# Kernel tuning notes

Hardware: AMD Instinct MI355X
Metric: run time of the kernel (lower is better)

## Reference

```python
import jax, jax.numpy as jnp
import numpy as np

N = 8192
D = 64  # node feature width
E = 64  # edge-derived feature width


def setup_inputs() -> dict:
    key = jax.random.key(0)
    k1, k2, k3 = jax.random.split(key, 3)
    # Dense normalized adjacency (module stores normalize(A).toarray()); values in [0,1).
    A = jax.random.uniform(k1, (N, N), dtype=jnp.float32) / N  # scaled like a normalized adjacency
    F = jax.random.normal(k2, (N, D), dtype=jnp.float32)
    new_features = jax.random.normal(k3, (N, E), dtype=jnp.float32)
    return {"A": A, "F": F, "new_features": new_features}


def reference(A, F, new_features):
    # layer 1: node branch gets ReLU, edge-feature branch does not
    h = jax.nn.relu(A @ F)              # [N, D]
    g = A @ new_features                # [N, E]
    # layer 2
    h = jax.nn.relu(A @ h)              # [N, D]
    g = A @ g                           # [N, E]
    return jnp.concatenate([h, g], axis=-1)  # [N, D+E]
```

## Files before the change

kernel.cpp:

```cpp
#include <hip/hip_runtime.h>
#include <hip/hip_bf16.h>


typedef unsigned short ushort_t;
typedef __attribute__((ext_vector_type(8))) short short8;
typedef __attribute__((ext_vector_type(4))) float f32x4;
typedef __attribute__((ext_vector_type(4))) unsigned short us4;

#define NN 8192
#define NO 128
#define NSPLIT 8
#define KSPAN 1024
#define KSTEPS 32

__global__ void detect_dtype(const ushort_t* __restrict__ A, int* __restrict__ flag) {
  __shared__ int smax, szero;
  const int t = threadIdx.x;
  if (t == 0) { smax = 0; szero = 0; }
  __syncthreads();
  int lmax = 0, lzero = 0;
  #pragma unroll
  for (int j = 0; j < 8; ++j) {
    int idx = t * 8 + j;
    int u = (int)A[idx];
    if ((idx & 1) == 0) {
      lmax = max(lmax, u);
      lzero += (u == 0) ? 1 : 0;
    }
  }
  atomicMax(&smax, lmax);
  atomicAdd(&szero, lzero);
  __syncthreads();
  if (t == 0) *flag = (smax > 0x3A00 || szero > 800) ? 1 : 0;
}

__global__ void zero_ws(float* __restrict__ p) {
  size_t i = ((size_t)blockIdx.x * 256 + threadIdx.x) * 4;
  *(float4*)(p + i) = make_float4(0.f, 0.f, 0.f, 0.f);
}

__device__ __forceinline__ short bf16bits(float x) {
  __hip_bfloat16 h = __float2bfloat16(x);
  return *reinterpret_cast<short*>(&h);
}

__device__ __forceinline__ short8 cvt8(float4 a, float4 b) {
  short8 r;
  r[0] = bf16bits(a.x); r[1] = bf16bits(a.y); r[2] = bf16bits(a.z); r[3] = bf16bits(a.w);
  r[4] = bf16bits(b.x); r[5] = bf16bits(b.y); r[6] = bf16bits(b.z); r[7] = bf16bits(b.w);
  return r;
}

__global__ void pack_b(const ushort_t* __restrict__ F, const ushort_t* __restrict__ NF,
                       ushort_t* __restrict__ Bpk, const int* __restrict__ flag) {
  int gid = blockIdx.x * 256 + threadIdx.x;
  int l = gid & 63, ks = (gid >> 6) & 255, nt = gid >> 14;
  int n = nt * 16 + (l & 15);
  int k0 = ks * 32 + (l >> 4) * 8;
  ushort_t* dst = Bpk + (((size_t)nt * 256 + ks) << 9) + l * 8;
  short8 v;
  if (*flag) {
    const float* src = (n < 64) ? ((const float*)F + n) : ((const float*)NF + n - 64);
    #pragma unroll
    for (int j = 0; j < 8; ++j) v[j] = bf16bits(src[(size_t)(k0 + j) << 6]);
  } else {
    const ushort_t* src = (n < 64) ? (F + n) : (NF + n - 64);
    #pragma unroll
    for (int j = 0; j < 8; ++j) v[j] = (short)src[(size_t)(k0 + j) << 6];
  }
  *(short8*)dst = v;
}

__global__ __launch_bounds__(256) void gemm(
    const ushort_t* __restrict__ Au, const float* __restrict__ Af,
    ushort_t* __restrict__ Apk, const ushort_t* __restrict__ Bpk,
    float* __restrict__ P, const int* __restrict__ flag, int wb, int usepk) {
  __shared__ __align__(16) ushort_t lsA[4 * 512];
  const int t = threadIdx.x;
  const int w = t >> 6, lane = t & 63;
  const int mblk = blockIdx.x >> 3;
  const int split = blockIdx.x & 7;
  const size_t m0 = (size_t)mblk * 64;
  const int ks0 = split * KSTEPS;
  const int l15 = lane & 15, lq = lane >> 4;
  const int fl = *flag;

  const f32x4 zero = {0.f, 0.f, 0.f, 0.f};
  f32x4 acc[8];
  #pragma unroll
  for (int nt = 0; nt < 8; ++nt) acc[nt] = zero;

  if (usepk && fl) {
    const ushort_t* ap = Apk + (((size_t)(mblk * 4 + w) * 256 + ks0) << 9) + lane * 8;
    const ushort_t* bp = Bpk + ((size_t)ks0 << 9) + lane * 8;
    #pragma unroll 2
    for (int it = 0; it < KSTEPS; ++it) {
      short8 a = *(const short8*)ap;
      #pragma unroll
      for (int nt = 0; nt < 8; ++nt) {
        short8 b = *(const short8*)(bp + ((size_t)nt << 17));
        acc[nt] = __builtin_amdgcn_mfma_f32_16x16x32_bf16(a, b, acc[nt], 0, 0, 0);
      }
      ap += 512; bp += 512;
    }
  } else {
    const int r = t >> 2, cq = t & 3;
    const int mt = r >> 4;
    const int li = (r & 15) + cq * 16;
    const float*    ap_f = Af + (m0 + r) * NN + (size_t)ks0 * 32 + cq * 8;
    const ushort_t* ap_b = Au + (m0 + r) * NN + (size_t)ks0 * 32 + cq * 8;
    ushort_t* wp = Apk + (((size_t)(mblk * 4 + mt) * 256 + ks0) << 9) + li * 8;
    ushort_t* lw = lsA + mt * 512 + li * 8;
    const ushort_t* lr = lsA + w * 512 + lane * 8;
    const int dowb = wb && fl;
    for (int it = 0; it < KSTEPS; ++it) {
      short8 c;
      if (fl) {
        float4 x0 = *(const float4*)ap_f;
        float4 x1 = *(const float4*)(ap_f + 4);
        c = cvt8(x0, x1);
        ap_f += 32;
      } else {
        c = *(const short8*)ap_b;
        ap_b += 32;
      }
      if (dowb) { *(short8*)wp = c; wp += 512; }
      const ushort_t* bit = Bpk + ((size_t)(ks0 + it) << 9) + lane * 8;
      __syncthreads();
      *(short8*)lw = c;
      __syncthreads();
      short8 a = *(const short8*)lr;
      #pragma unroll
      for (int nt = 0; nt < 8; ++nt) {
        short8 b = *(const short8*)(bit + ((size_t)nt << 17));
        acc[nt] = __builtin_amdgcn_mfma_f32_16x16x32_bf16(a, b, acc[nt], 0, 0, 0);
      }
    }
  }

  const size_t mrow = m0 + w * 16 + lq * 4;
  #pragma unroll
  for (int nt = 0; nt < 8; ++nt) {
    #pragma unroll
    for (int reg = 0; reg < 4; ++reg) {
      unsafeAtomicAdd(&P[(mrow + reg) * NO + nt * 16 + l15], acc[nt][reg]);
    }
  }
}

__global__ void epi_pack(const float* __restrict__ P, ushort_t* __restrict__ Bpk2) {
  __shared__ ushort_t lt[64 * 130];
  const int t = threadIdx.x;
  const int blk = blockIdx.x;
  const size_t base = (size_t)blk * 64 * NO;
  #pragma unroll
  for (int i = 0; i < 8; ++i) {
    int e4 = (i * 256 + t) * 4;
    int m = e4 >> 7, n = e4 & 127;
    float4 v = *(const float4*)(P + base + e4);
    float s[4] = {v.x, v.y, v.z, v.w};
    if (n < 64) {
      #pragma unroll
      for (int j = 0; j < 4; ++j) s[j] = fmaxf(s[j], 0.f);
    }
    #pragma unroll
    for (int j = 0; j < 4; ++j) lt[m * 130 + n + j] = (ushort_t)bf16bits(s[j]);
  }
  __syncthreads();
  #pragma unroll
  for (int i = 0; i < 4; ++i) {
    int item = i * 256 + t;
    int l = item & 63, s = (item >> 6) & 1, nt = item >> 7;
    short8 v;
    #pragma unroll
    for (int j = 0; j < 8; ++j)
      v[j] = (short)lt[(s * 32 + (l >> 4) * 8 + j) * 130 + nt * 16 + (l & 15)];
    *(short8*)(Bpk2 + (((size_t)nt * 256 + blk * 2 + s) << 9) + l * 8) = v;
  }
}

__global__ void epi_out(const float* __restrict__ P, ushort_t* __restrict__ outb,
                        float* __restrict__ outf, const int* __restrict__ flag) {
  int idx = blockIdx.x * 256 + threadIdx.x;
  size_t e = (size_t)idx * 4;
  float4 v = *(const float4*)(P + e);
  float s[4] = {v.x, v.y, v.z, v.w};
  int n0 = (int)(e & 127);
  #pragma unroll
  for (int j = 0; j < 4; ++j) if (n0 + j < 64) s[j] = fmaxf(s[j], 0.f);
  if (*flag) {
    *(float4*)(outf + e) = make_float4(s[0], s[1], s[2], s[3]);
  } else {
    us4 r;
    #pragma unroll
    for (int j = 0; j < 4; ++j) r[j] = (ushort_t)bf16bits(s[j]);
    *(us4*)(outb + e) = r;
  }
}

extern "C" void kernel_launch(void* const* d_in, const int* in_sizes, int n_in,
                              void* d_out, int out_size, void* d_ws, size_t ws_size,
                              hipStream_t stream) {
  const ushort_t* A  = (const ushort_t*)d_in[0];
  const ushort_t* F  = (const ushort_t*)d_in[1];
  const ushort_t* NF = (const ushort_t*)d_in[2];

  char* ws = (char*)d_ws;
  ushort_t* Bpk1 = (ushort_t*)(ws);
  ushort_t* Bpk2 = (ushort_t*)(ws + (2u << 20));
  float*    P1   = (float*)(ws + (4u << 20));
  float*    P2   = (float*)(ws + (8u << 20));
  int*      flag = (int*)(ws + (12u << 20));
  ushort_t* Apk  = (ushort_t*)(ws + (16u << 20));

  const int wsok = (ws_size >= ((size_t)144 << 20) + 4) ? 1 : 0;

  detect_dtype<<<1, 256, 0, stream>>>(A, flag);
  zero_ws<<<2048, 256, 0, stream>>>(P1);
  pack_b<<<512, 256, 0, stream>>>(F, NF, Bpk1, flag);
  gemm<<<1024, 256, 0, stream>>>(A, (const float*)A, Apk, Bpk1, P1, flag,
                                 wsok, 0);
  epi_pack<<<128, 256, 0, stream>>>(P1, Bpk2);
  gemm<<<1024, 256, 0, stream>>>(A, (const float*)A, Apk, Bpk2, P2, flag,
                                 0, wsok);
  epi_out<<<1024, 256, 0, stream>>>(P2, (ushort_t*)d_out, (float*)d_out, flag);
}
```

Baseline: 514.2 us.

## Fuse split-K reduction and epilogues into GEMM via in-block LDS reduction

Each block now owns 16 output rows, and its four waves split K among themselves instead of spreading split-K across blocks. Partial results are reduced in shared memory rather than with global float atomics. The ReLU, bf16 packing for the second layer, and the final output write move into the GEMM epilogue, which removes the zero, epi_pack and epi_out launches and the fp32 partial buffers. The A tile is staged per wave in 64KB of swizzled LDS. The large LDS footprint limits occupancy, and the grid shrinks to 512 blocks.

After: 505.5 us. Within noise of the previous version (-1.7%).

```diff
diff --git a/kernel.cpp b/kernel.cpp
--- a/kernel.cpp
+++ b/kernel.cpp
@@ -9,9 +9,6 @@
 
 #define NN 8192
 #define NO 128
-#define NSPLIT 8
-#define KSPAN 1024
-#define KSTEPS 32
 
 __global__ void detect_dtype(const ushort_t* __restrict__ A, int* __restrict__ flag) {
   __shared__ int smax, szero;
@@ -34,21 +31,9 @@
   if (t == 0) *flag = (smax > 0x3A00 || szero > 800) ? 1 : 0;
 }
 
-__global__ void zero_ws(float* __restrict__ p) {
-  size_t i = ((size_t)blockIdx.x * 256 + threadIdx.x) * 4;
-  *(float4*)(p + i) = make_float4(0.f, 0.f, 0.f, 0.f);
-}
-
 __device__ __forceinline__ short bf16bits(float x) {
   __hip_bfloat16 h = __float2bfloat16(x);
   return *reinterpret_cast<short*>(&h);
-}
-
-__device__ __forceinline__ short8 cvt8(float4 a, float4 b) {
-  short8 r;
-  r[0] = bf16bits(a.x); r[1] = bf16bits(a.y); r[2] = bf16bits(a.z); r[3] = bf16bits(a.w);
-  r[4] = bf16bits(b.x); r[5] = bf16bits(b.y); r[6] = bf16bits(b.z); r[7] = bf16bits(b.w);
-  return r;
 }
 
 __global__ void pack_b(const ushort_t* __restrict__ F, const ushort_t* __restrict__ NF,
@@ -74,14 +59,13 @@
 __global__ __launch_bounds__(256) void gemm(
     const ushort_t* __restrict__ Au, const float* __restrict__ Af,
     ushort_t* __restrict__ Apk, const ushort_t* __restrict__ Bpk,
-    float* __restrict__ P, const int* __restrict__ flag, int wb, int usepk) {
-  __shared__ __align__(16) ushort_t lsA[4 * 512];
+    ushort_t* __restrict__ Bpk2, ushort_t* __restrict__ outb,
+    float* __restrict__ outf, const int* __restrict__ flag,
+    int wb, int usepk, int outmode) {
+  __shared__ __align__(16) char lds[65536];
   const int t = threadIdx.x;
   const int w = t >> 6, lane = t & 63;
-  const int mblk = blockIdx.x >> 3;
-  const int split = blockIdx.x & 7;
-  const size_t m0 = (size_t)mblk * 64;
-  const int ks0 = split * KSTEPS;
+  const int b = blockIdx.x;
   const int l15 = lane & 15, lq = lane >> 4;
   const int fl = *flag;
 
@@ -91,110 +75,104 @@
   for (int nt = 0; nt < 8; ++nt) acc[nt] = zero;
 
   if (usepk && fl) {
-    const ushort_t* ap = Apk + (((size_t)(mblk * 4 + w) * 256 + ks0) << 9) + lane * 8;
-    const ushort_t* bp = Bpk + ((size_t)ks0 << 9) + lane * 8;
+    const ushort_t* ap = Apk + (((size_t)b * 256 + w * 64) << 9) + lane * 8;
+    const ushort_t* bp = Bpk + (((size_t)w * 64) << 9) + lane * 8;
     #pragma unroll 2
-    for (int it = 0; it < KSTEPS; ++it) {
-      short8 a = *(const short8*)ap;
+    for (int kk = 0; kk < 64; ++kk) {
+      short8 a = *(const short8*)(ap + ((size_t)kk << 9));
       #pragma unroll
       for (int nt = 0; nt < 8; ++nt) {
-        short8 b = *(const short8*)(bp + ((size_t)nt << 17));
-        acc[nt] = __builtin_amdgcn_mfma_f32_16x16x32_bf16(a, b, acc[nt], 0, 0, 0);
+        short8 bfr = *(const short8*)(bp + ((size_t)nt << 17) + ((size_t)kk << 9));
+        acc[nt] = __builtin_amdgcn_mfma_f32_16x16x32_bf16(a, bfr, acc[nt], 0, 0, 0);
       }
-      ap += 512; bp += 512;
     }
   } else {
-    const int r = t >> 2, cq = t & 3;
-    const int mt = r >> 4;
-    const int li = (r & 15) + cq * 16;
-    const float*    ap_f = Af + (m0 + r) * NN + (size_t)ks0 * 32 + cq * 8;
-    const ushort_t* ap_b = Au + (m0 + r) * NN + (size_t)ks0 * 32 + cq * 8;
-    ushort_t* wp = Apk + (((size_t)(mblk * 4 + mt) * 256 + ks0) << 9) + li * 8;
-    ushort_t* lw = lsA + mt * 512 + li * 8;
-    const ushort_t* lr = lsA + w * 512 + lane * 8;
+    char* myA = lds + w * 16384;
+    const size_t row0 = (size_t)b * 16;
     const int dowb = wb && fl;
-    for (int it = 0; it < KSTEPS; ++it) {
-      short8 c;
+    for (int s = 0; s < 4; ++s) {
+      const int k0 = w * 2048 + s * 512;
       if (fl) {
-        float4 x0 = *(const float4*)ap_f;
-        float4 x1 = *(const float4*)(ap_f + 4);
-        c = cvt8(x0, x1);
-        ap_f += 32;
+        #pragma unroll 4
+        for (int r = 0; r < 16; ++r) {
+          const float* src = Af + (row0 + r) * NN + k0 + lane * 4;
+          float4 x0 = *(const float4*)src;
+          float4 x1 = *(const float4*)(src + 256);
+          const int swz = (r & 7) << 4;
+          us4 v0, v1;
+          v0[0] = (ushort_t)bf16bits(x0.x); v0[1] = (ushort_t)bf16bits(x0.y);
+          v0[2] = (ushort_t)bf16bits(x0.z); v0[3] = (ushort_t)bf16bits(x0.w);
+          v1[0] = (ushort_t)bf16bits(x1.x); v1[1] = (ushort_t)bf16bits(x1.y);
+          v1[2] = (ushort_t)bf16bits(x1.z); v1[3] = (ushort_t)bf16bits(x1.w);
+          *(us4*)(myA + r * 1024 + ((lane * 8) ^ swz)) = v0;
+          *(us4*)(myA + r * 1024 + ((512 + lane * 8) ^ swz)) = v1;
+        }
       } else {
-        c = *(const short8*)ap_b;
-        ap_b += 32;
+        #pragma unroll 4
+        for (int r = 0; r < 16; ++r) {
+          short8 x = *(const short8*)(Au + (row0 + r) * NN + k0 + lane * 8);
+          const int swz = (r & 7) << 4;
+          *(short8*)(myA + r * 1024 + ((lane * 16) ^ swz)) = x;
+        }
       }
-      if (dowb) { *(short8*)wp = c; wp += 512; }
-      const ushort_t* bit = Bpk + ((size_t)(ks0 + it) << 9) + lane * 8;
-      __syncthreads();
-      *(short8*)lw = c;
-      __syncthreads();
-      short8 a = *(const short8*)lr;
+      #pragma unroll 2
+      for (int kk = 0; kk < 16; ++kk) {
+        short8 a = *(const short8*)(myA + l15 * 1024 +
+                                    (((kk * 64) + lq * 16) ^ ((l15 & 7) << 4)));
+        const int ks = w * 64 + s * 16 + kk;
+        if (dowb)
+          *(short8*)(Apk + (((size_t)b * 256 + ks) << 9) + lane * 8) = a;
+        const ushort_t* bp = Bpk + ((size_t)ks << 9) + lane * 8;
+        #pragma unroll
+        for (int nt = 0; nt < 8; ++nt) {
+          short8 bfr = *(const short8*)(bp + ((size_t)nt << 17));
+          acc[nt] = __builtin_amdgcn_mfma_f32_16x16x32_bf16(a, bfr, acc[nt], 0, 0, 0);
+        }
+      }
+    }
+  }
+
+  __syncthreads();
+  float* red = (float*)lds;
+  #pragma unroll
+  for (int nt = 0; nt < 8; ++nt) {
+    #pragma unroll
+    for (int reg = 0; reg < 4; ++reg)
+      red[w * 2048 + (lq * 4 + reg) * 128 + nt * 16 + l15] = acc[nt][reg];
+  }
+  __syncthreads();
+  const int i = t * 8;
+  const int m = t >> 4, n0 = (t & 15) * 8;
+  float s8[8];
+  #pragma unroll
+  for (int j = 0; j < 8; ++j)
+    s8[j] = red[i + j] + red[2048 + i + j] + red[4096 + i + j] + red[6144 + i + j];
+  if (n0 < 64) {
+    #pragma unroll
+    for (int j = 0; j < 8; ++j) s8[j] = fmaxf(s8[j], 0.f);
+  }
+
+  if (outmode == 0) {
+    const int ks = b >> 1, hs = b & 1;
+    #pragma unroll
+    for (int j = 0; j < 8; ++j) {
+      const int n = n0 + j;
+      const int nt = n >> 4;
+      const int ld = (n & 15) + ((m >> 3) + 2 * hs) * 16;
+      Bpk2[(((size_t)nt * 256 + ks) << 9) + ld * 8 + (m & 7)] =
+          (ushort_t)bf16bits(s8[j]);
+    }
+  } else {
+    const size_t e = (size_t)b * 2048 + i;
+    if (fl) {
+      *(float4*)(outf + e)     = make_float4(s8[0], s8[1], s8[2], s8[3]);
+      *(float4*)(outf + e + 4) = make_float4(s8[4], s8[5], s8[6], s8[7]);
+    } else {
+      short8 r;
       #pragma unroll
-      for (int nt = 0; nt < 8; ++nt) {
-        short8 b = *(const short8*)(bit + ((size_t)nt << 17));
-        acc[nt] = __builtin_amdgcn_mfma_f32_16x16x32_bf16(a, b, acc[nt], 0, 0, 0);
-      }
-    }
-  }
-
-  const size_t mrow = m0 + w * 16 + lq * 4;
-  #pragma unroll
-  for (int nt = 0; nt < 8; ++nt) {
-    #pragma unroll
-    for (int reg = 0; reg < 4; ++reg) {
-      unsafeAtomicAdd(&P[(mrow + reg) * NO + nt * 16 + l15], acc[nt][reg]);
-    }
-  }
-}
-
-__global__ void epi_pack(const float* __restrict__ P, ushort_t* __restrict__ Bpk2) {
-  __shared__ ushort_t lt[64 * 130];
-  const int t = threadIdx.x;
-  const int blk = blockIdx.x;
-  const size_t base = (size_t)blk * 64 * NO;
-  #pragma unroll
-  for (int i = 0; i < 8; ++i) {
-    int e4 = (i * 256 + t) * 4;
-    int m = e4 >> 7, n = e4 & 127;
-    float4 v = *(const float4*)(P + base + e4);
-    float s[4] = {v.x, v.y, v.z, v.w};
-    if (n < 64) {
-      #pragma unroll
-      for (int j = 0; j < 4; ++j) s[j] = fmaxf(s[j], 0.f);
-    }
-    #pragma unroll
-    for (int j = 0; j < 4; ++j) lt[m * 130 + n + j] = (ushort_t)bf16bits(s[j]);
-  }
-  __syncthreads();
-  #pragma unroll
-  for (int i = 0; i < 4; ++i) {
-    int item = i * 256 + t;
-    int l = item & 63, s = (item >> 6) & 1, nt = item >> 7;
-    short8 v;
-    #pragma unroll
-    for (int j = 0; j < 8; ++j)
-      v[j] = (short)lt[(s * 32 + (l >> 4) * 8 + j) * 130 + nt * 16 + (l & 15)];
-    *(short8*)(Bpk2 + (((size_t)nt * 256 + blk * 2 + s) << 9) + l * 8) = v;
-  }
-}
-
-__global__ void epi_out(const float* __restrict__ P, ushort_t* __restrict__ outb,
-                        float* __restrict__ outf, const int* __restrict__ flag) {
-  int idx = blockIdx.x * 256 + threadIdx.x;
-  size_t e = (size_t)idx * 4;
-  float4 v = *(const float4*)(P + e);
-  float s[4] = {v.x, v.y, v.z, v.w};
-  int n0 = (int)(e & 127);
-  #pragma unroll
-  for (int j = 0; j < 4; ++j) if (n0 + j < 64) s[j] = fmaxf(s[j], 0.f);
-  if (*flag) {
-    *(float4*)(outf + e) = make_float4(s[0], s[1], s[2], s[3]);
-  } else {
-    us4 r;
-    #pragma unroll
-    for (int j = 0; j < 4; ++j) r[j] = (ushort_t)bf16bits(s[j]);
-    *(us4*)(outb + e) = r;
+      for (int j = 0; j < 8; ++j) r[j] = bf16bits(s8[j]);
+      *(short8*)(outb + e) = r;
+    }
   }
 }
 
@@ -208,20 +186,16 @@
   char* ws = (char*)d_ws;
   ushort_t* Bpk1 = (ushort_t*)(ws);
   ushort_t* Bpk2 = (ushort_t*)(ws + (2u << 20));
-  float*    P1   = (float*)(ws + (4u << 20));
-  float*    P2   = (float*)(ws + (8u << 20));
-  int*      flag = (int*)(ws + (12u << 20));
-  ushort_t* Apk  = (ushort_t*)(ws + (16u << 20));
-
-  const int wsok = (ws_size >= ((size_t)144 << 20) + 4) ? 1 : 0;
+  int*      flag = (int*)(ws + (4u << 20));
+  ushort_t* Apk  = (ushort_t*)(ws + (8u << 20));
+
+  const int wsok = (ws_size >= ((size_t)144 << 20)) ? 1 : 0;
 
   detect_dtype<<<1, 256, 0, stream>>>(A, flag);
-  zero_ws<<<2048, 256, 0, stream>>>(P1);
   pack_b<<<512, 256, 0, stream>>>(F, NF, Bpk1, flag);
-  gemm<<<1024, 256, 0, stream>>>(A, (const float*)A, Apk, Bpk1, P1, flag,
-                                 wsok, 0);
-  epi_pack<<<128, 256, 0, stream>>>(P1, Bpk2);
-  gemm<<<1024, 256, 0, stream>>>(A, (const float*)A, Apk, Bpk2, P2, flag,
-                                 0, wsok);
-  epi_out<<<1024, 256, 0, stream>>>(P2, (ushort_t*)d_out, (float*)d_out, flag);
-}
+  gemm<<<512, 256, 0, stream>>>(A, (const float*)A, Apk, Bpk1, Bpk2,
+                                nullptr, nullptr, flag, wsok, 0, 0);
+  gemm<<<512, 256, 0, stream>>>(A, (const float*)A, Apk, Bpk2, Bpk2,
+                                (ushort_t*)d_out, (float*)d_out, flag,
+                                0, wsok, 1);
+}
```
